# Optimization experiments

Hardware: AMD Instinct MI355X
Metric: run time of the kernel (lower is better)

Reference implementation:

```python
import jax, jax.numpy as jnp
import numpy as np

N, E = 20000, 320000
IN_DIM, EDGE_DIM, HID = 64, 16, 64
# (in_c, heads, channels, out_c) per layer; last layer heads=1, concat=False
DIMS = [(64, 4, 64, 256), (256, 4, 64, 256), (256, 1, 64, 64)]


def _ln(x, g, b):
    m = x.mean(-1, keepdims=True)
    v = x.var(-1, keepdims=True)
    return (x - m) / jnp.sqrt(v + 1e-5) * g + b


def _gatv2(x, ei, ea, Wl, bl, Wr, br, We, att, bc, concat):
    # PyG GATv2Conv, eval mode (no dropout), add_self_loops=True, fill_value='mean'
    n = x.shape[0]
    H, C = att.shape
    ar = jnp.arange(n, dtype=ei.dtype)
    src = jnp.concatenate([ei[0], ar])
    dst = jnp.concatenate([ei[1], ar])
    ea_f = jnp.concatenate([ea, jnp.broadcast_to(ea.mean(0), (n, ea.shape[1]))], 0)
    xl = (x @ Wl + bl).reshape(n, H, C)   # source transform
    xr = (x @ Wr + br).reshape(n, H, C)   # target transform
    ee = (ea_f @ We).reshape(-1, H, C)    # edge transform (no bias in PyG)
    e = jax.nn.leaky_relu(xl[src] + xr[dst] + ee, 0.2)       # [E+N, H, C]
    score = jnp.einsum('ehc,hc->eh', e, att)                 # [E+N, H]
    mx = jax.ops.segment_max(score, dst, num_segments=n)
    a = jnp.exp(score - mx[dst])
    a = a / (jax.ops.segment_sum(a, dst, num_segments=n)[dst] + 1e-16)
    out = jax.ops.segment_sum(a[:, :, None] * xl[src], dst, num_segments=n)  # [N,H,C]
    out = out.reshape(n, H * C) if concat else out.mean(1)
    return out + bc


def _forward(x, eis, eas, Wp, bp, gp, bep, layers):
    h = jax.nn.gelu(_ln(x @ Wp + bp, gp, bep), approximate=False)
    for i in range(3):
        Wl, bl, Wr, br, We, att, bc, g, be, Wsk, bsk = layers[i]
        res = h @ Wsk + bsk
        h = _gatv2(h, eis[i], eas[i], Wl, bl, Wr, br, We, att, bc, i < 2)
        h = jax.nn.gelu(_ln(h, g, be), approximate=False) + res
    return h


def setup_inputs() -> dict:
    key = jax.random.key(0)
    ks = iter(jax.random.split(key, 64))
    rn = lambda shape, s=0.05: jax.random.normal(next(ks), shape, jnp.float32) * s
    d = {'x': jax.random.normal(next(ks), (N, IN_DIM), jnp.float32)}
    for i in range(3):
        d['ei%d' % i] = jax.random.randint(next(ks), (2, E), 0, N, jnp.int32)
        d['ea%d' % i] = jax.random.normal(next(ks), (E, EDGE_DIM), jnp.float32)
    d['Wp'] = rn((IN_DIM, HID)); d['bp'] = jnp.zeros(HID)
    d['gp'] = jnp.ones(HID); d['bep'] = jnp.zeros(HID)
    for i, (ic, H, C, oc) in enumerate(DIMS):
        hc = H * C
        d['Wl%d' % i] = rn((ic, hc)); d['bl%d' % i] = jnp.zeros(hc)
        d['Wr%d' % i] = rn((ic, hc)); d['br%d' % i] = jnp.zeros(hc)
        d['We%d' % i] = rn((EDGE_DIM, hc))
        d['att%d' % i] = rn((H, C), 0.1)
        d['bc%d' % i] = jnp.zeros(hc if i < 2 else C)
        d['g%d' % i] = jnp.ones(oc); d['be%d' % i] = jnp.zeros(oc)
        d['Wsk%d' % i] = rn((ic, oc)); d['bsk%d' % i] = jnp.zeros(oc)
    return d


def reference(x, ei0, ea0, ei1, ea1, ei2, ea2, Wp, bp, gp, bep,
              Wl0, bl0, Wr0, br0, We0, att0, bc0, g0, be0, Wsk0, bsk0,
              Wl1, bl1, Wr1, br1, We1, att1, bc1, g1, be1, Wsk1, bsk1,
              Wl2, bl2, Wr2, br2, We2, att2, bc2, g2, be2, Wsk2, bsk2):
    layers = [
        (Wl0, bl0, Wr0, br0, We0, att0, bc0, g0, be0, Wsk0, bsk0),
        (Wl1, bl1, Wr1, br1, We1, att1, bc1, g1, be1, Wsk1, bsk1),
        (Wl2, bl2, Wr2, br2, We2, att2, bc2, g2, be2, Wsk2, bsk2),
    ]
    return _forward(x, (ei0, ei1, ei2), (ea0, ea1, ea2), Wp, bp, gp, bep, layers)
```

## Files before the change

kernel.cpp:

```cpp
#include <hip/hip_runtime.h>
#include <hip/hip_bf16.h>
#include <math.h>

#define NV 20000
#define NE 320000
#define CSR_PAD 16

typedef __attribute__((ext_vector_type(8))) short bf16x8;
typedef __attribute__((ext_vector_type(4))) float f32x4;
typedef __attribute__((ext_vector_type(2))) _Float16 h2;

static __device__ __forceinline__ ushort f2b(float f) {
  __hip_bfloat16 h = __float2bfloat16(f);
  return *reinterpret_cast<ushort*>(&h);
}
static __device__ __forceinline__ float b2f(ushort u) {
  union { ushort s[2]; float f; } c;
  c.s[0] = 0; c.s[1] = u;
  return c.f;
}
static __device__ __forceinline__ ushort f2h(float f) {
  _Float16 h = (_Float16)f;
  return *reinterpret_cast<ushort*>(&h);
}
static __device__ __forceinline__ float blo(unsigned u) { return __uint_as_float(u << 16); }
static __device__ __forceinline__ float bhi(unsigned u) { return __uint_as_float(u & 0xffff0000u); }

static __device__ __forceinline__ float wave_sum64(float x) {
  x += __int_as_float(__builtin_amdgcn_update_dpp(0, __float_as_int(x), 0x111, 0xF, 0xF, true));
  x += __int_as_float(__builtin_amdgcn_update_dpp(0, __float_as_int(x), 0x112, 0xF, 0xF, true));
  x += __int_as_float(__builtin_amdgcn_update_dpp(0, __float_as_int(x), 0x114, 0xF, 0xF, true));
  x += __int_as_float(__builtin_amdgcn_update_dpp(0, __float_as_int(x), 0x118, 0xF, 0xF, true));
  x += __int_as_float(__builtin_amdgcn_update_dpp(0, __float_as_int(x), 0x142, 0xA, 0xF, true));
  x += __int_as_float(__builtin_amdgcn_update_dpp(0, __float_as_int(x), 0x143, 0xC, 0xF, true));
  return __int_as_float(__builtin_amdgcn_readlane(__float_as_int(x), 63));
}

static __device__ __forceinline__ float sum16(float x) {
  x += __int_as_float(__builtin_amdgcn_update_dpp(0, __float_as_int(x), 0x121, 0xF, 0xF, true));
  x += __int_as_float(__builtin_amdgcn_update_dpp(0, __float_as_int(x), 0x122, 0xF, 0xF, true));
  x += __int_as_float(__builtin_amdgcn_update_dpp(0, __float_as_int(x), 0x124, 0xF, 0xF, true));
  x += __int_as_float(__builtin_amdgcn_update_dpp(0, __float_as_int(x), 0x128, 0xF, 0xF, true));
  return x;
}

static __device__ __forceinline__ float dot16h(const uint4* __restrict__ E,
                                               const h2* __restrict__ Wch) {
#if __has_builtin(__builtin_amdgcn_fdot2)
  const h2* e = (const h2*)E;
  float s = 0.f;
#pragma unroll
  for (int j = 0; j < 8; ++j) s = __builtin_amdgcn_fdot2(e[j], Wch[j], s, false);
  return s;
#else
  const unsigned* u = (const unsigned*)E;
  float s = 0.f;
#pragma unroll
  for (int j = 0; j < 8; ++j) {
    union { unsigned v; h2 h; } cv; cv.v = u[j];
    s = fmaf((float)cv.h[0], (float)Wch[j][0], s);
    s = fmaf((float)cv.h[1], (float)Wch[j][1], s);
  }
  return s;
#endif
}

struct CJob { const float* src; ushort* dst; int K, M; };
struct PrepArgs {
  const int* ei[3];
  const float* ea[3];
  int* counts[3];
  float* easum[3];
  ushort* eab[3];
  CJob jobs[9];
  const float *x, *Wp, *bp, *gp, *bep;
  ushort* h0;
};

__global__ __launch_bounds__(256) void prep_kernel(PrepArgs a) {
  const int y = blockIdx.y, t = threadIdx.x;
  if (y < 3) {
    if (blockIdx.x < 256) {
      const float4* ea4 = (const float4*)a.ea[y];
      ushort* eab = a.eab[y];
      const int cg = t & 3;
      int r = blockIdx.x * 64 + (t >> 2);
      const int rstride = 256 * 64;
      float4 s = make_float4(0.f, 0.f, 0.f, 0.f);
      for (; r < NE; r += rstride) {
        float4 v = ea4[(size_t)r * 4 + cg];
        s.x += v.x; s.y += v.y; s.z += v.z; s.w += v.w;
        uint2 w;
        w.x = (unsigned)f2h(v.x) | ((unsigned)f2h(v.y) << 16);
        w.y = (unsigned)f2h(v.z) | ((unsigned)f2h(v.w) << 16);
        *(uint2*)(eab + (size_t)r * 16 + cg * 4) = w;
      }
      __shared__ float4 red4[256];
      red4[t] = s;
      __syncthreads();
      if (t < 4) {
        float4 tot = make_float4(0.f, 0.f, 0.f, 0.f);
        for (int j = t; j < 256; j += 4) {
          float4 v = red4[j];
          tot.x += v.x; tot.y += v.y; tot.z += v.z; tot.w += v.w;
        }
        atomicAdd(&a.easum[y][t * 4 + 0], tot.x);
        atomicAdd(&a.easum[y][t * 4 + 1], tot.y);
        atomicAdd(&a.easum[y][t * 4 + 2], tot.z);
        atomicAdd(&a.easum[y][t * 4 + 3], tot.w);
      }
    }
    int i = blockIdx.x * 256 + t;
    if (i < NE) atomicAdd(&a.counts[y][a.ei[y][NE + i]], 1);
  } else if (y == 3) {
#pragma unroll
    for (int j = 0; j < 9; ++j) {
      CJob jb = a.jobs[j];
      const int total = jb.M * jb.K;
      for (int i = blockIdx.x * 256 + t; i < total; i += gridDim.x * 256) {
        int m = i / jb.K, k = i - m * jb.K;
        jb.dst[i] = f2b(jb.src[(size_t)k * jb.M + m]);
      }
    }
  } else {
    int wid = t >> 6, lane = t & 63;
    for (int row = blockIdx.x * 4 + wid; row < NV; row += gridDim.x * 4) {
      float xv = a.x[(size_t)row * 64 + lane];
      float acc = a.bp[lane];
#pragma unroll
      for (int k = 0; k < 64; ++k) {
        float v = __shfl(xv, k, 64);
        acc = fmaf(v, a.Wp[k * 64 + lane], acc);
      }
      float s1 = wave_sum64(acc), s2 = wave_sum64(acc * acc);
      float mean = s1 * (1.0f / 64.0f);
      float var  = s2 * (1.0f / 64.0f) - mean * mean;
      float yv = (acc - mean) * rsqrtf(var + 1e-5f) * a.gp[lane] + a.bep[lane];
      float gel = 0.5f * yv * (1.0f + erff(yv * 0.70710678118654752f));
      a.h0[(size_t)row * 64 + lane] = f2b(gel);
    }
  }
}

__global__ __launch_bounds__(1024) void scan_kernel(
    int* __restrict__ countsA, int* __restrict__ cursorA)
{
  int* counts = countsA + blockIdx.x * (NV + 1);
  int* cursor = cursorA + blockIdx.x * NV;
  __shared__ int ws[16];
  __shared__ int wexcl[17];
  const int t = threadIdx.x, lane = t & 63, wid = t >> 6;
  const int base = t * 20;
  int v[20];
  int tot = 0;
#pragma unroll
  for (int j = 0; j < 20; ++j) {
    int i = base + j;
    v[j] = (i < NV) ? counts[i] : 0;
    tot += v[j];
  }
  int x = tot;
#pragma unroll
  for (int o = 1; o < 64; o <<= 1) {
    int yy = __shfl_up(x, o, 64);
    if (lane >= o) x += yy;
  }
  if (lane == 63) ws[wid] = x;
  __syncthreads();
  if (t == 0) {
    int r = 0;
#pragma unroll
    for (int j = 0; j < 16; ++j) { wexcl[j] = r; r += ws[j]; }
    wexcl[16] = r;
  }
  __syncthreads();
  int run = wexcl[wid] + (x - tot);
#pragma unroll
  for (int j = 0; j < 20; ++j) {
    int i = base + j;
    if (i < NV) { counts[i] = run; cursor[i] = run; }
    run += v[j];
  }
  if (t == 0) counts[NV] = wexcl[16];
}

struct G0SArgs {
  const ushort *A, *WT;
  const float *b0, *b1, *b2;
  ushort *O0, *O1; float* O2;
  int K, M1, M2, Mtot, NT;
  const int* ei[3];
  int* cursor;
  uint2* csr[3]; int HC[3];
};

__global__ __launch_bounds__(256) void gemm0_scatter_kernel(G0SArgs a) {
  __shared__ ushort As[128][40];
  __shared__ ushort Bs[64][40];
  const int t = threadIdx.x;
  if ((int)blockIdx.x < a.NT) {
    const int wave = t >> 6, lane = t & 63;
    const int mcols = a.Mtot >> 6;
    const int col0 = ((int)blockIdx.x % mcols) * 64, row0 = ((int)blockIdx.x / mcols) * 128;
    const int m_ = lane & 15, q = lane >> 4;
    f32x4 acc[2][4];
#pragma unroll
    for (int i = 0; i < 2; ++i)
#pragma unroll
      for (int j = 0; j < 4; ++j) acc[i][j] = (f32x4){0.f, 0.f, 0.f, 0.f};
    const int ar = t >> 1, ac = (t & 1) * 16;
    const int br = t >> 2, bcol = (t & 3) * 8;
    const ushort* Ap = a.A + (size_t)(row0 + ar) * a.K + ac;
    const ushort* Bp = a.WT + (size_t)(col0 + br) * a.K + bcol;
    const bool a_ok = (row0 + ar) < NV;
    for (int k0 = 0; k0 < a.K; k0 += 32) {
      uint4 av0 = make_uint4(0, 0, 0, 0), av1 = make_uint4(0, 0, 0, 0);
      if (a_ok) { av0 = *(const uint4*)(Ap + k0); av1 = *(const uint4*)(Ap + k0 + 8); }
      uint4 bv = *(const uint4*)(Bp + k0);
      *(uint4*)&As[ar][ac] = av0;
      *(uint4*)&As[ar][ac + 8] = av1;
      *(uint4*)&Bs[br][bcol] = bv;
      __syncthreads();
      bf16x8 a0 = *(const bf16x8*)&As[wave * 32 + m_][q * 8];
      bf16x8 a1 = *(const bf16x8*)&As[wave * 32 + 16 + m_][q * 8];
#pragma unroll
      for (int cf = 0; cf < 4; ++cf) {
        bf16x8 b = *(const bf16x8*)&Bs[cf * 16 + m_][q * 8];
        acc[0][cf] = __builtin_amdgcn_mfma_f32_16x16x32_bf16(a0, b, acc[0][cf], 0, 0, 0);
        acc[1][cf] = __builtin_amdgcn_mfma_f32_16x16x32_bf16(a1, b, acc[1][cf], 0, 0, 0);
      }
      __syncthreads();
    }
    const float* bias; int base, mode, Wd;
    if (col0 < a.M1)      { bias = a.b0; base = 0;    mode = 0; Wd = a.M1; }
    else if (col0 < a.M2) { bias = a.b1; base = a.M1; mode = 1; Wd = a.M2 - a.M1; }
    else                  { bias = a.b2; base = a.M2; mode = 2; Wd = a.Mtot - a.M2; }
#pragma unroll
    for (int rf = 0; rf < 2; ++rf) {
#pragma unroll
      for (int cf = 0; cf < 4; ++cf) {
        int col = col0 + cf * 16 + m_ - base;
        float bb = bias[col];
#pragma unroll
        for (int r = 0; r < 4; ++r) {
          int row = row0 + wave * 32 + rf * 16 + q * 4 + r;
          if (row < NV) {
            float v = acc[rf][cf][r] + bb;
            if (mode == 0)      a.O0[(size_t)row * Wd + col] = f2b(v);
            else if (mode == 1) a.O1[(size_t)row * Wd + col] = f2b(v);
            else                a.O2[(size_t)row * Wd + col] = v;
          }
        }
      }
    }
  } else {
    const int per = NE + CSR_PAD;
    int gi = ((int)blockIdx.x - a.NT) * 256 + t;
    if (gi >= 3 * per) return;
    int l = gi / per, i = gi - l * per;
    if (i >= NE) {
      a.csr[l][i] = make_uint2(0u, 0u);
      return;
    }
    int dst = a.ei[l][NE + i], src = a.ei[l][i];
    int pos = atomicAdd(&a.cursor[(size_t)l * NV + dst], 1);
    a.csr[l][pos] = make_uint2((unsigned)(src * a.HC[l]), (unsigned)i);
  }
}

__global__ __launch_bounds__(256) void gemm_fused(
    const ushort* __restrict__ A, const ushort* __restrict__ WT,
    const float* __restrict__ b0, const float* __restrict__ b1,
    const float* __restrict__ b2,
    ushort* __restrict__ O0, ushort* __restrict__ O1, float* __restrict__ O2,
    int N, int K, int M1, int M2, int Mtot)
{
  __shared__ ushort As[128][40];
  __shared__ ushort Bs[64][40];
  const int t = threadIdx.x, wave = t >> 6, lane = t & 63;
  const int row0 = blockIdx.y * 128, col0 = blockIdx.x * 64;
  const int m_ = lane & 15, q = lane >> 4;
  f32x4 acc[2][4];
#pragma unroll
  for (int i = 0; i < 2; ++i)
#pragma unroll
    for (int j = 0; j < 4; ++j) acc[i][j] = (f32x4){0.f, 0.f, 0.f, 0.f};
  const int ar = t >> 1, ac = (t & 1) * 16;
  const int br = t >> 2, bcol = (t & 3) * 8;
  const ushort* Ap = A + (size_t)(row0 + ar) * K + ac;
  const ushort* Bp = WT + (size_t)(col0 + br) * K + bcol;
  const bool a_ok = (row0 + ar) < N;
  for (int k0 = 0; k0 < K; k0 += 32) {
    uint4 av0 = make_uint4(0, 0, 0, 0), av1 = make_uint4(0, 0, 0, 0);
    if (a_ok) { av0 = *(const uint4*)(Ap + k0); av1 = *(const uint4*)(Ap + k0 + 8); }
    uint4 bv = *(const uint4*)(Bp + k0);
    *(uint4*)&As[ar][ac] = av0;
    *(uint4*)&As[ar][ac + 8] = av1;
    *(uint4*)&Bs[br][bcol] = bv;
    __syncthreads();
    bf16x8 a0 = *(const bf16x8*)&As[wave * 32 + m_][q * 8];
    bf16x8 a1 = *(const bf16x8*)&As[wave * 32 + 16 + m_][q * 8];
#pragma unroll
    for (int cf = 0; cf < 4; ++cf) {
      bf16x8 b = *(const bf16x8*)&Bs[cf * 16 + m_][q * 8];
      acc[0][cf] = __builtin_amdgcn_mfma_f32_16x16x32_bf16(a0, b, acc[0][cf], 0, 0, 0);
      acc[1][cf] = __builtin_amdgcn_mfma_f32_16x16x32_bf16(a1, b, acc[1][cf], 0, 0, 0);
    }
    __syncthreads();
  }
  const float* bias; int base, mode, Wd;
  if (col0 < M1)      { bias = b0; base = 0;  mode = 0; Wd = M1; }
  else if (col0 < M2) { bias = b1; base = M1; mode = 1; Wd = M2 - M1; }
  else                { bias = b2; base = M2; mode = 2; Wd = Mtot - M2; }
#pragma unroll
  for (int rf = 0; rf < 2; ++rf) {
#pragma unroll
    for (int cf = 0; cf < 4; ++cf) {
      int col = col0 + cf * 16 + m_ - base;
      float bb = bias[col];
#pragma unroll
      for (int r = 0; r < 4; ++r) {
        int row = row0 + wave * 32 + rf * 16 + q * 4 + r;
        if (row < N) {
          float v = acc[rf][cf][r] + bb;
          if (mode == 0)      O0[(size_t)row * Wd + col] = f2b(v);
          else if (mode == 1) O1[(size_t)row * Wd + col] = f2b(v);
          else                O2[(size_t)row * Wd + col] = v;
        }
      }
    }
  }
}

__global__ __launch_bounds__(256) void agg4_kernel(
    const ushort* __restrict__ eab, const float* __restrict__ easum,
    const float* __restrict__ We,
    const ushort* __restrict__ xl, const ushort* __restrict__ xr,
    const float* __restrict__ att, const float* __restrict__ bc,
    const float* __restrict__ g, const float* __restrict__ be,
    const float* __restrict__ res,
    const int* __restrict__ offs, const uint2* __restrict__ csr,
    ushort* __restrict__ houtb, int E)
{
  const int t = threadIdx.x, lane = t & 63, wave = t >> 6;
  const int n = blockIdx.x * 4 + wave;
  const int cb = 4 * lane;
  const size_t rowb = (size_t)n * 256 + cb;
  const float L2E = 1.4426950408889634f;

  float4 atv = *(const float4*)(att + cb);
  float at[4] = {atv.x * L2E, atv.y * L2E, atv.z * L2E, atv.w * L2E};

  h2 Wch[4][8];
  float esf[4] = {0.f, 0.f, 0.f, 0.f};
#pragma unroll
  for (int k = 0; k < 8; ++k) {
    float4 wr0 = *(const float4*)(We + (2 * k) * 256 + cb);
    float4 wr1 = *(const float4*)(We + (2 * k + 1) * 256 + cb);
    const float* w0 = &wr0.x;
    const float* w1 = &wr1.x;
    float e0 = easum[2 * k], e1 = easum[2 * k + 1];
#pragma unroll
    for (int j = 0; j < 4; ++j) {
      esf[j] = fmaf(e0, w0[j], esf[j]);
      esf[j] = fmaf(e1, w1[j], esf[j]);
      Wch[j][k] = (h2){(_Float16)w0[j], (_Float16)w1[j]};
    }
  }
#pragma unroll
  for (int j = 0; j < 4; ++j) esf[j] *= 1.0f / (float)E;

  uint2 qr = *(const uint2*)(xr + rowb);
  float xrv[4] = {blo(qr.x), bhi(qr.x), blo(qr.y), bhi(qr.y)};
  uint2 qn = *(const uint2*)(xl + rowb);
  float xln[4] = {blo(qn.x), bhi(qn.x), blo(qn.y), bhi(qn.y)};

  float p = 0.f;
#pragma unroll
  for (int j = 0; j < 4; ++j) {
    float v = xln[j] + xrv[j] + esf[j];
    v = v > 0.f ? v : 0.2f * v;
    p = fmaf(v, at[j], p);
  }
  float wself = exp2f(sum16(p));
  float acc[4];
#pragma unroll
  for (int j = 0; j < 4; ++j) acc[j] = wself * xln[j];
  float denom = wself;

  const int beg = __builtin_amdgcn_readfirstlane(offs[n]);
  const int end = __builtin_amdgcn_readfirstlane(offs[n + 1]);

  uint2 QS[2];
  uint4 EA[2][2];
  uint2 XL[2];
  {
    uint2 Q0[2];
#pragma unroll
    for (int k = 0; k < 2; ++k) Q0[k] = csr[beg + k];
#pragma unroll
    for (int k = 0; k < 2; ++k) QS[k] = csr[beg + 2 + k];
#pragma unroll
    for (int k = 0; k < 2; ++k) {
      const uint4* ep = (const uint4*)(eab +
          (size_t)__builtin_amdgcn_readfirstlane(Q0[k].y) * 16);
      EA[k][0] = ep[0]; EA[k][1] = ep[1];
      XL[k] = *(const uint2*)(xl + __builtin_amdgcn_readfirstlane(Q0[k].x) + cb);
    }
  }

  for (int idx = beg; idx < end; idx += 2) {
    uint2 QN[2];
#pragma unroll
    for (int k = 0; k < 2; ++k) QN[k] = csr[idx + 4 + k];
    uint4 EB[2][2];
    uint2 XN[2];
#pragma unroll
    for (int k = 0; k < 2; ++k) {
      const uint4* ep = (const uint4*)(eab +
          (size_t)__builtin_amdgcn_readfirstlane(QS[k].y) * 16);
      EB[k][0] = ep[0]; EB[k][1] = ep[1];
      XN[k] = *(const uint2*)(xl + __builtin_amdgcn_readfirstlane(QS[k].x) + cb);
    }

#pragma unroll
    for (int k = 0; k < 2; ++k) {
      float xf[4] = {blo(XL[k].x), bhi(XL[k].x), blo(XL[k].y), bhi(XL[k].y)};
      float pp = 0.f;
#pragma unroll
      for (int j = 0; j < 4; ++j) {
        float ee = dot16h(EA[k], Wch[j]);
        float v = xf[j] + xrv[j] + ee;
        v = v > 0.f ? v : 0.2f * v;
        pp = fmaf(v, at[j], pp);
      }
      float S = sum16(pp);
      float w = (idx + k < end) ? exp2f(S) : 0.f;
#pragma unroll
      for (int j = 0; j < 4; ++j) acc[j] = fmaf(w, xf[j], acc[j]);
      denom += w;
    }
#pragma unroll
    for (int k = 0; k < 2; ++k) {
      EA[k][0] = EB[k][0]; EA[k][1] = EB[k][1]; XL[k] = XN[k]; QS[k] = QN[k];
    }
  }

  const float inv = 1.0f / (denom + 1e-16f);
  float4 bcv = *(const float4*)(bc + cb);
  float out[4];
  out[0] = acc[0] * inv + bcv.x; out[1] = acc[1] * inv + bcv.y;
  out[2] = acc[2] * inv + bcv.z; out[3] = acc[3] * inv + bcv.w;

  float so1 = out[0] + out[1] + out[2] + out[3];
  float so2 = out[0] * out[0] + out[1] * out[1] + out[2] * out[2] + out[3] * out[3];
  float s1 = wave_sum64(so1), s2 = wave_sum64(so2);
  float mean = s1 * (1.0f / 256.0f);
  float var  = s2 * (1.0f / 256.0f) - mean * mean;
  float rstd = rsqrtf(var + 1e-5f);
  float4 gv = *(const float4*)(g + cb);
  float4 bev = *(const float4*)(be + cb);
  float4 rv = *(const float4*)(res + rowb);
  const float* gp = &gv.x; const float* bep = &bev.x; const float* rp = &rv.x;
  ushort ob[4];
#pragma unroll
  for (int j = 0; j < 4; ++j) {
    float y = (out[j] - mean) * rstd * gp[j] + bep[j];
    float gel = 0.5f * y * (1.0f + erff(y * 0.70710678118654752f));
    ob[j] = f2b(gel + rp[j]);
  }
  uint2 ov;
  ov.x = (unsigned)ob[0] | ((unsigned)ob[1] << 16);
  ov.y = (unsigned)ob[2] | ((unsigned)ob[3] << 16);
  *(uint2*)(houtb + rowb) = ov;
}

__global__ __launch_bounds__(256, 4) void agg1_kernel(
    const ushort* __restrict__ eab, const float* __restrict__ easum,
    const float* __restrict__ We,
    const ushort* __restrict__ xl, const ushort* __restrict__ xr,
    const float* __restrict__ att, const float* __restrict__ bc,
    const float* __restrict__ g, const float* __restrict__ be,
    const float* __restrict__ res,
    const int* __restrict__ offs, const uint2* __restrict__ csr,
    float* __restrict__ houtf, int E)
{
  const int HC = 64;
  const int t = threadIdx.x, lane = t & 63, wave = t >> 6;
  const int n = blockIdx.x * 4 + wave;
  const int c = lane;

  const float xr_t = b2f(xr[(size_t)n * HC + c]);
  const float att_t = att[c] * 1.4426950408889634f;
  float eself = 0.f;
  h2 Wch[8];
#pragma unroll
  for (int j = 0; j < 8; ++j) {
    float w0 = We[(2 * j) * HC + c], w1 = We[(2 * j + 1) * HC + c];
    eself = fmaf(easum[2 * j], w0, eself);
    eself = fmaf(easum[2 * j + 1], w1, eself);
    Wch[j] = (h2){(_Float16)w0, (_Float16)w1};
  }
  eself *= 1.0f / (float)E;

  const float xln = b2f(xl[(size_t)n * HC + c]);
  float vs = xln + xr_t + eself;
  vs = vs > 0.f ? vs : 0.2f * vs;
  const float wself = exp2f(wave_sum64(vs * att_t));
  float acc = wself * xln, denom = wself;

  const int beg = __builtin_amdgcn_readfirstlane(offs[n]);
  const int end = __builtin_amdgcn_readfirstlane(offs[n + 1]);

  uint2 QS[4];
  uint4 EA[4][2];
  float XL[4];
  {
    uint2 Q0[4];
#pragma unroll
    for (int k = 0; k < 4; ++k) Q0[k] = csr[beg + k];
#pragma unroll
    for (int k = 0; k < 4; ++k) QS[k] = csr[beg + 4 + k];
#pragma unroll
    for (int k = 0; k < 4; ++k) {
      const uint4* ep = (const uint4*)(eab +
          (size_t)__builtin_amdgcn_readfirstlane(Q0[k].y) * 16);
      EA[k][0] = ep[0]; EA[k][1] = ep[1];
    }
#pragma unroll
    for (int k = 0; k < 4; ++k)
      XL[k] = b2f(xl[__builtin_amdgcn_readfirstlane(Q0[k].x) + c]);
  }

  for (int idx = beg; idx < end; idx += 4) {
    uint2 QN[4];
#pragma unroll
    for (int k = 0; k < 4; ++k) QN[k] = csr[idx + 8 + k];
    uint4 EB[4][2];
    float XLN[4];
#pragma unroll
    for (int k = 0; k < 4; ++k) {
      const uint4* ep = (const uint4*)(eab +
          (size_t)__builtin_amdgcn_readfirstlane(QS[k].y) * 16);
      EB[k][0] = ep[0]; EB[k][1] = ep[1];
    }
#pragma unroll
    for (int k = 0; k < 4; ++k)
      XLN[k] = b2f(xl[__builtin_amdgcn_readfirstlane(QS[k].x) + c]);

    float wv[4];
#pragma unroll
    for (int k = 0; k < 4; ++k) {
      float ee = dot16h(EA[k], Wch);
      float v = XL[k] + xr_t + ee;
      v = v > 0.f ? v : 0.2f * v;
      float S = wave_sum64(v * att_t);
      wv[k] = (idx + k < end) ? exp2f(S) : 0.f;
    }
#pragma unroll
    for (int k = 0; k < 4; ++k) { acc = fmaf(wv[k], XL[k], acc); denom += wv[k]; }
#pragma unroll
    for (int k = 0; k < 4; ++k) {
      EA[k][0] = EB[k][0]; EA[k][1] = EB[k][1]; XL[k] = XLN[k]; QS[k] = QN[k];
    }
  }

  float out = acc / (denom + 1e-16f) + bc[c];
  float s1 = wave_sum64(out), s2 = wave_sum64(out * out);
  float mean = s1 / (float)HC;
  float var  = s2 / (float)HC - mean * mean;
  float y = (out - mean) * rsqrtf(var + 1e-5f) * g[c] + be[c];
  float gel = 0.5f * y * (1.0f + erff(y * 0.70710678118654752f));
  houtf[(size_t)n * HC + c] = gel + res[(size_t)n * HC + c];
}

extern "C" void kernel_launch(void* const* d_in, const int* in_sizes, int n_in,
                              void* d_out, int out_size, void* d_ws, size_t ws_size,
                              hipStream_t stream)
{
  auto in = [&](int i) { return (const float*)d_in[i]; };

  const int ic[3] = {64, 256, 256}, hc[3] = {256, 256, 64}, oc[3] = {256, 256, 64};
  const int CSRN = NE + CSR_PAD;

  char* w = (char*)d_ws;
  size_t off = 0;
  auto alloc = [&](size_t bytes) { void* p = w + off; off = (off + bytes + 511) & ~(size_t)511; return p; };
  ushort* B1   = (ushort*)alloc((size_t)NV * 256 * 2);
  ushort* B2   = (ushort*)alloc((size_t)NV * 256 * 2);
  float*  B3   = (float*)alloc((size_t)NV * 256 * 4);
  ushort* h0bf = (ushort*)alloc((size_t)NV * 64 * 2);
  ushort* h1bf = (ushort*)alloc((size_t)NV * 256 * 2);
  ushort* h2bf = (ushort*)alloc((size_t)NV * 256 * 2);
  ushort* Wcat[3];
  for (int i = 0; i < 3; ++i)
    Wcat[i] = (ushort*)alloc((size_t)(2 * hc[i] + oc[i]) * ic[i] * 2);
  float*    easumA  = (float*)alloc(3 * 64);
  int*      countsA = (int*)alloc((size_t)3 * (NV + 1) * 4);
  int*      cursorA = (int*)alloc((size_t)3 * NV * 4);
  uint2*    csr2A   = (uint2*)alloc((size_t)3 * CSRN * sizeof(uint2));
  ushort*   eab16A  = (ushort*)alloc((size_t)3 * NE * 16 * 2);

  hipMemsetAsync(easumA, 0, 512 + (size_t)3 * (NV + 1) * 4, stream);

  PrepArgs pa;
  for (int i = 0; i < 3; ++i) {
    pa.ei[i] = (const int*)d_in[1 + 2 * i];
    pa.ea[i] = in(2 + 2 * i);
    pa.counts[i] = countsA + i * (NV + 1);
    pa.easum[i] = easumA + i * 16;
    pa.eab[i] = eab16A + (size_t)i * NE * 16;
    pa.jobs[i * 3 + 0] = {in(11 + 11 * i), Wcat[i],                             ic[i], hc[i]};
    pa.jobs[i * 3 + 1] = {in(13 + 11 * i), Wcat[i] + (size_t)hc[i] * ic[i],     ic[i], hc[i]};
    pa.jobs[i * 3 + 2] = {in(20 + 11 * i), Wcat[i] + (size_t)2 * hc[i] * ic[i], ic[i], oc[i]};
  }
  pa.x = in(0); pa.Wp = in(7); pa.bp = in(8); pa.gp = in(9); pa.bep = in(10);
  pa.h0 = h0bf;
  prep_kernel<<<dim3(1344, 5), 256, 0, stream>>>(pa);

  scan_kernel<<<3, 1024, 0, stream>>>(countsA, cursorA);

  G0SArgs ga;
  ga.A = h0bf; ga.WT = Wcat[0];
  ga.b0 = in(12); ga.b1 = in(14); ga.b2 = in(21);
  ga.O0 = B1; ga.O1 = B2; ga.O2 = B3;
  ga.K = 64; ga.M1 = 256; ga.M2 = 512; ga.Mtot = 768;
  ga.NT = (768 / 64) * ((NV + 127) / 128);
  for (int i = 0; i < 3; ++i) {
    ga.ei[i] = (const int*)d_in[1 + 2 * i];
    ga.csr[i] = csr2A + (size_t)i * CSRN;
    ga.HC[i] = hc[i];
  }
  ga.cursor = cursorA;
  const int scat_blocks = (3 * (NE + CSR_PAD) + 255) / 256;
  gemm0_scatter_kernel<<<ga.NT + scat_blocks, 256, 0, stream>>>(ga);

  agg4_kernel<<<NV / 4, 256, 0, stream>>>(
      eab16A, easumA + 0, in(15), B1, B2, in(16), in(17), in(18), in(19),
      B3, countsA, csr2A, h1bf, NE);

  gemm_fused<<<dim3(768 / 64, (NV + 127) / 128), 256, 0, stream>>>(
      h1bf, Wcat[1], in(23), in(25), in(32), B1, B2, B3, NV, 256, 256, 512, 768);

  agg4_kernel<<<NV / 4, 256, 0, stream>>>(
      eab16A + (size_t)NE * 16, easumA + 16, in(26), B1, B2, in(27), in(28),
      in(29), in(30), B3, countsA + (NV + 1), csr2A + (size_t)CSRN, h2bf, NE);

  gemm_fused<<<dim3(192 / 64, (NV + 127) / 128), 256, 0, stream>>>(
      h2bf, Wcat[2], in(34), in(36), in(43), B1, B2, B3, NV, 256, 64, 128, 192);

  agg1_kernel<<<NV / 4, 256, 0, stream>>>(
      eab16A + (size_t)2 * NE * 16, easumA + 32, in(37), B1, B2, in(38), in(39),
      in(40), in(41), B3, countsA + 2 * (NV + 1), csr2A + (size_t)2 * CSRN,
      (float*)d_out, NE);
}
```

Measured before the change: 564.5 us.

## Privatize degree counts and partition CSR scatter by destination octant

Degree counting now spreads atomics across eight private count arrays chosen by block index, and the scan kernel sums them into a separate offsets array. The CSR scatter is restructured so each block scans a chunk of edges but only inserts those whose destination falls in one of eight node ranges, which localises cursor atomics and CSR writes. The edge-attribute conversion also uses twice as many blocks. The cost is eight times more count memory to clear and reduce, and each edge index is read eight times during the scatter.

Measured after the change: 621.0 us. +10.0%, slower.

```diff
diff --git a/kernel.cpp b/kernel.cpp
--- a/kernel.cpp
+++ b/kernel.cpp
@@ -5,6 +5,9 @@
 #define NV 20000
 #define NE 320000
 #define CSR_PAD 16
+#define NOCT 8
+#define OCTW (NV / NOCT)
+#define SCAT_B 64
 
 typedef __attribute__((ext_vector_type(8))) short bf16x8;
 typedef __attribute__((ext_vector_type(4))) float f32x4;
@@ -80,12 +83,12 @@
 __global__ __launch_bounds__(256) void prep_kernel(PrepArgs a) {
   const int y = blockIdx.y, t = threadIdx.x;
   if (y < 3) {
-    if (blockIdx.x < 256) {
+    if (blockIdx.x < 512) {
       const float4* ea4 = (const float4*)a.ea[y];
       ushort* eab = a.eab[y];
       const int cg = t & 3;
       int r = blockIdx.x * 64 + (t >> 2);
-      const int rstride = 256 * 64;
+      const int rstride = 512 * 64;
       float4 s = make_float4(0.f, 0.f, 0.f, 0.f);
       for (; r < NE; r += rstride) {
         float4 v = ea4[(size_t)r * 4 + cg];
@@ -111,7 +114,8 @@
       }
     }
     int i = blockIdx.x * 256 + t;
-    if (i < NE) atomicAdd(&a.counts[y][a.ei[y][NE + i]], 1);
+    if (i < NE)
+      atomicAdd(&a.counts[y][(blockIdx.x & 7) * (NV + 1) + a.ei[y][NE + i]], 1);
   } else if (y == 3) {
 #pragma unroll
     for (int j = 0; j < 9; ++j) {
@@ -143,9 +147,11 @@
 }
 
 __global__ __launch_bounds__(1024) void scan_kernel(
-    int* __restrict__ countsA, int* __restrict__ cursorA)
+    const int* __restrict__ countsA, int* __restrict__ offsA,
+    int* __restrict__ cursorA)
 {
-  int* counts = countsA + blockIdx.x * (NV + 1);
+  const int* counts = countsA + blockIdx.x * NOCT * (NV + 1);
+  int* offs = offsA + blockIdx.x * (NV + 1);
   int* cursor = cursorA + blockIdx.x * NV;
   __shared__ int ws[16];
   __shared__ int wexcl[17];
@@ -156,8 +162,13 @@
 #pragma unroll
   for (int j = 0; j < 20; ++j) {
     int i = base + j;
-    v[j] = (i < NV) ? counts[i] : 0;
-    tot += v[j];
+    int c = 0;
+    if (i < NV) {
+#pragma unroll
+      for (int o = 0; o < NOCT; ++o) c += counts[o * (NV + 1) + i];
+    }
+    v[j] = c;
+    tot += c;
   }
   int x = tot;
 #pragma unroll
@@ -178,10 +189,10 @@
 #pragma unroll
   for (int j = 0; j < 20; ++j) {
     int i = base + j;
-    if (i < NV) { counts[i] = run; cursor[i] = run; }
+    if (i < NV) { offs[i] = run; cursor[i] = run; }
     run += v[j];
   }
-  if (t == 0) counts[NV] = wexcl[16];
+  if (t == 0) offs[NV] = wexcl[16];
 }
 
 struct G0SArgs {
@@ -254,17 +265,28 @@
       }
     }
   } else {
-    const int per = NE + CSR_PAD;
-    int gi = ((int)blockIdx.x - a.NT) * 256 + t;
-    if (gi >= 3 * per) return;
-    int l = gi / per, i = gi - l * per;
-    if (i >= NE) {
-      a.csr[l][i] = make_uint2(0u, 0u);
-      return;
-    }
-    int dst = a.ei[l][NE + i], src = a.ei[l][i];
-    int pos = atomicAdd(&a.cursor[(size_t)l * NV + dst], 1);
-    a.csr[l][pos] = make_uint2((unsigned)(src * a.HC[l]), (unsigned)i);
+    const int sb = (int)blockIdx.x - a.NT;
+    const int r = sb % 24;
+    const int l = r >> 3, o = r & 7;
+    const int b = sb / 24;
+    if (o == 0 && b == 0 && t < CSR_PAD)
+      a.csr[l][NE + t] = make_uint2(0u, 0u);
+    const int lo = o * OCTW, hi = lo + OCTW;
+    const int chunk = (NE + SCAT_B - 1) / SCAT_B;
+    const int i0 = b * chunk;
+    const int i1 = (i0 + chunk < NE) ? i0 + chunk : NE;
+    const int* dstp = a.ei[l] + NE;
+    const int* srcp = a.ei[l];
+    int* cur = a.cursor + (size_t)l * NV;
+    uint2* csr = a.csr[l];
+    const int hc = a.HC[l];
+    for (int i = i0 + t; i < i1; i += 256) {
+      int d = dstp[i];
+      if (d >= lo && d < hi) {
+        int pos = atomicAdd(&cur[d], 1);
+        csr[pos] = make_uint2((unsigned)(srcp[i] * hc), (unsigned)i);
+      }
+    }
   }
 }
 
@@ -596,18 +618,19 @@
   for (int i = 0; i < 3; ++i)
     Wcat[i] = (ushort*)alloc((size_t)(2 * hc[i] + oc[i]) * ic[i] * 2);
   float*    easumA  = (float*)alloc(3 * 64);
-  int*      countsA = (int*)alloc((size_t)3 * (NV + 1) * 4);
+  int*      countsA = (int*)alloc((size_t)3 * NOCT * (NV + 1) * 4);
+  int*      offsA   = (int*)alloc((size_t)3 * (NV + 1) * 4);
   int*      cursorA = (int*)alloc((size_t)3 * NV * 4);
   uint2*    csr2A   = (uint2*)alloc((size_t)3 * CSRN * sizeof(uint2));
   ushort*   eab16A  = (ushort*)alloc((size_t)3 * NE * 16 * 2);
 
-  hipMemsetAsync(easumA, 0, 512 + (size_t)3 * (NV + 1) * 4, stream);
+  hipMemsetAsync(easumA, 0, 512 + (size_t)3 * NOCT * (NV + 1) * 4, stream);
 
   PrepArgs pa;
   for (int i = 0; i < 3; ++i) {
     pa.ei[i] = (const int*)d_in[1 + 2 * i];
     pa.ea[i] = in(2 + 2 * i);
-    pa.counts[i] = countsA + i * (NV + 1);
+    pa.counts[i] = countsA + (size_t)i * NOCT * (NV + 1);
     pa.easum[i] = easumA + i * 16;
     pa.eab[i] = eab16A + (size_t)i * NE * 16;
     pa.jobs[i * 3 + 0] = {in(11 + 11 * i), Wcat[i],                             ic[i], hc[i]};
@@ -618,7 +641,7 @@
   pa.h0 = h0bf;
   prep_kernel<<<dim3(1344, 5), 256, 0, stream>>>(pa);
 
-  scan_kernel<<<3, 1024, 0, stream>>>(countsA, cursorA);
+  scan_kernel<<<3, 1024, 0, stream>>>(countsA, offsA, cursorA);
 
   G0SArgs ga;
   ga.A = h0bf; ga.WT = Wcat[0];
@@ -632,25 +655,25 @@
     ga.HC[i] = hc[i];
   }
   ga.cursor = cursorA;
-  const int scat_blocks = (3 * (NE + CSR_PAD) + 255) / 256;
+  const int scat_blocks = 3 * NOCT * SCAT_B;
   gemm0_scatter_kernel<<<ga.NT + scat_blocks, 256, 0, stream>>>(ga);
 
   agg4_kernel<<<NV / 4, 256, 0, stream>>>(
       eab16A, easumA + 0, in(15), B1, B2, in(16), in(17), in(18), in(19),
-      B3, countsA, csr2A, h1bf, NE);
+      B3, offsA, csr2A, h1bf, NE);
 
   gemm_fused<<<dim3(768 / 64, (NV + 127) / 128), 256, 0, stream>>>(
       h1bf, Wcat[1], in(23), in(25), in(32), B1, B2, B3, NV, 256, 256, 512, 768);
 
   agg4_kernel<<<NV / 4, 256, 0, stream>>>(
       eab16A + (size_t)NE * 16, easumA + 16, in(26), B1, B2, in(27), in(28),
-      in(29), in(30), B3, countsA + (NV + 1), csr2A + (size_t)CSRN, h2bf, NE);
+      in(29), in(30), B3, offsA + (NV + 1), csr2A + (size_t)CSRN, h2bf, NE);
 
   gemm_fused<<<dim3(192 / 64, (NV + 127) / 128), 256, 0, stream>>>(
       h2bf, Wcat[2], in(34), in(36), in(43), B1, B2, B3, NV, 256, 64, 128, 192);
 
   agg1_kernel<<<NV / 4, 256, 0, stream>>>(
       eab16A + (size_t)2 * NE * 16, easumA + 32, in(37), B1, B2, in(38), in(39),
-      in(40), in(41), B3, countsA + 2 * (NV + 1), csr2A + (size_t)2 * CSRN,
+      in(40), in(41), B3, offsA + 2 * (NV + 1), csr2A + (size_t)2 * CSRN,
       (float*)d_out, NE);
 }
```
